# Performance work log

Hardware: AMD Instinct MI355X
Metric: run time of the kernel (lower is better)

## Reference

```python
import jax, jax.numpy as jnp
import numpy as np

D_ATTN = 64


def setup_inputs() -> dict:
    key = jax.random.key(0)
    ks = jax.random.split(key, 10)
    B, N, D_MODEL = 8, 1024, 512
    s = 0.02
    return {
        "x": jax.random.normal(ks[0], (B, N, D_MODEL), jnp.float32),
        "top": jax.random.normal(ks[1], (B, N, N, 16), jnp.float32),
        "Wq": jax.random.normal(ks[2], (D_MODEL, D_ATTN), jnp.float32) * s,
        "bq": jnp.zeros((D_ATTN,), jnp.float32),
        "Wk": jax.random.normal(ks[3], (D_MODEL, D_ATTN), jnp.float32) * s,
        "bk": jnp.zeros((D_ATTN,), jnp.float32),
        "Wv": jax.random.normal(ks[4], (D_MODEL, D_ATTN), jnp.float32) * s,
        "bv": jnp.zeros((D_ATTN,), jnp.float32),
        "Wt": jax.random.normal(ks[5], (16, 1), jnp.float32) * s,
        "bt": jnp.zeros((1,), jnp.float32),
    }


def reference(x, top, Wq, bq, Wk, bk, Wv, bv, Wt, bt):
    # QKV projections: [B,N,d_model] -> [B,N,d_attn]
    Q = x @ Wq + bq
    K = x @ Wk + bk
    V = x @ Wv + bv
    scale = 1.0 / jnp.sqrt(jnp.asarray(D_ATTN, x.dtype))
    # [B,N,N] attention logits
    logits = jnp.einsum("bnd,bmd->bnm", Q, K) * scale
    # learned topological bias: Linear(16,1) on [B,N,N,16] -> [B,N,N]
    bias = jnp.einsum("bnmf,fo->bnmo", top, Wt)[..., 0] + bt[0]
    score = jax.nn.softmax(logits + bias, axis=-1)
    return jnp.einsum("bnm,bmd->bnd", score, V)
```

## Files before the change

kernel.cpp:

```cpp
#include <hip/hip_runtime.h>
#include <hip/hip_bf16.h>

typedef __attribute__((ext_vector_type(8))) short short8;
typedef __attribute__((ext_vector_type(4))) float f32x4;
typedef unsigned short ushort_t;
typedef unsigned int uint_t;

#define D_MODEL 512
#define D_ATTN  64

__device__ __forceinline__ ushort_t f2bf(float f) {
    uint_t u = __float_as_uint(f);
    u += 0x7FFFu + ((u >> 16) & 1u);
    return (ushort_t)(u >> 16);
}
__device__ __forceinline__ f32x4 ntload4(const f32x4* p) {
    return __builtin_nontemporal_load(p);
}

__global__ __launch_bounds__(256)
void qkv_all(const float* __restrict__ x,
             const float* __restrict__ Wq, const float* __restrict__ bq,
             const float* __restrict__ Wk, const float* __restrict__ bk,
             const float* __restrict__ Wv, const float* __restrict__ bv,
             ushort_t* __restrict__ Q, ushort_t* __restrict__ K,
             ushort_t* __restrict__ Vt)
{
    const int l = threadIdx.x & 63, w = threadIdx.x >> 6;
    const size_t bn0 = (size_t)blockIdx.x << 4;
    const int r0 = w << 2;
    const float* xb = x + (bn0 + r0) * D_MODEL;
    { uintptr_t u = (uintptr_t)xb; asm volatile("" : "+v"(u)); xb = (const float*)u; }

    float aq[4] = {0,0,0,0}, ak[4] = {0,0,0,0}, av[4] = {0,0,0,0};
#pragma unroll 2
    for (int k = 0; k < D_MODEL; k += 4) {
        float4 xr[4];
#pragma unroll
        for (int r = 0; r < 4; ++r) xr[r] = *(const float4*)(xb + r * D_MODEL + k);
        float wqv[4], wkv[4], wvv[4];
#pragma unroll
        for (int kk = 0; kk < 4; ++kk) {
            wqv[kk] = Wq[(k + kk) * D_ATTN + l];
            wkv[kk] = Wk[(k + kk) * D_ATTN + l];
            wvv[kk] = Wv[(k + kk) * D_ATTN + l];
        }
#pragma unroll
        for (int r = 0; r < 4; ++r) {
            const float xv[4] = {xr[r].x, xr[r].y, xr[r].z, xr[r].w};
#pragma unroll
            for (int kk = 0; kk < 4; ++kk) {
                aq[r] = fmaf(xv[kk], wqv[kk], aq[r]);
                ak[r] = fmaf(xv[kk], wkv[kk], ak[r]);
                av[r] = fmaf(xv[kk], wvv[kk], av[r]);
            }
        }
    }
    const float bqv = bq[l], bkv = bk[l], bvv = bv[l];
#pragma unroll
    for (int r = 0; r < 4; ++r) {
        Q[(bn0 + r0 + r) * D_ATTN + l] = f2bf((aq[r] + bqv) * 0.125f);
        K[(bn0 + r0 + r) * D_ATTN + l] = f2bf(ak[r] + bkv);
    }
    const int b = (int)(bn0 >> 10), n0loc = (int)(bn0 & 1023);
    uint2 pv;
    pv.x = (uint_t)f2bf(av[0] + bvv) | ((uint_t)f2bf(av[1] + bvv) << 16);
    pv.y = (uint_t)f2bf(av[2] + bvv) | ((uint_t)f2bf(av[3] + bvv) << 16);
    *(uint2*)(Vt + ((size_t)(b * 64 + l) << 10) + n0loc + r0) = pv;
}

__global__ __launch_bounds__(256)
void topo_attn_f(const float* __restrict__ top, const float* __restrict__ Wt,
                 const ushort_t* __restrict__ Q, const ushort_t* __restrict__ K,
                 const ushort_t* __restrict__ Vt, float* __restrict__ out)
{
    __shared__ float lds[16384];
    const int tid = threadIdx.x;
    const int l = tid & 63, wv = tid >> 6;
    const int b   = blockIdx.x >> 6;
    const int bn0 = blockIdx.x << 4;

    {
        const f32x4* __restrict__ slab =
            (const f32x4*)top + ((size_t)bn0 << 12) + ((size_t)wv << 14) + l;
        const float4 wq = *(const float4*)(Wt + ((l & 3) << 2));
        const int mq = l >> 2;
        const bool sel0 = (l & 3) == 0;
#pragma unroll 1
        for (int bi = 0; bi < 16; ++bi) {
            f32x4 ld[16];
#pragma unroll
            for (int u = 0; u < 16; ++u)
                ld[u] = ntload4(slab + (((bi << 4) + u) << 6));
#pragma unroll
            for (int u = 0; u < 16; ++u) {
                int j = (bi << 4) + u;
                float p = ld[u][0] * wq.x;
                p = fmaf(ld[u][1], wq.y, p);
                p = fmaf(ld[u][2], wq.z, p);
                p = fmaf(ld[u][3], wq.w, p);
                p += __shfl_xor(p, 1);
                p += __shfl_xor(p, 2);
                int m_slab = (j << 4) + mq;
                int rloc = (wv << 2) + (m_slab >> 10);
                int m = m_slab & 1023;
                if (sel0) lds[rloc * 1024 + m] = p;
            }
        }
    }
    __syncthreads();

    const int lr = l & 15, lg = l >> 4;
    const short8 a0 = *(const short8*)(Q + ((size_t)(bn0 + lr)) * 64 + 8 * lg);
    const short8 a1 = *(const short8*)(Q + ((size_t)(bn0 + lr)) * 64 + 32 + 8 * lg);
    const ushort_t* __restrict__ Kb = K + ((size_t)b << 16);
#pragma unroll 4
    for (int t16 = 0; t16 < 16; ++t16) {
        int m0 = (wv << 8) + (t16 << 4);
        short8 kb0 = *(const short8*)(Kb + (size_t)(m0 + lr) * 64 + 8 * lg);
        short8 kb1 = *(const short8*)(Kb + (size_t)(m0 + lr) * 64 + 32 + 8 * lg);
        f32x4 acc = {0.f, 0.f, 0.f, 0.f};
        acc = __builtin_amdgcn_mfma_f32_16x16x32_bf16(a0, kb0, acc, 0, 0, 0);
        acc = __builtin_amdgcn_mfma_f32_16x16x32_bf16(a1, kb1, acc, 0, 0, 0);
#pragma unroll
        for (int j = 0; j < 4; ++j)
            lds[(4 * lg + j) * 1024 + m0 + lr] += acc[j];
    }
    __syncthreads();

    {
        const int r = tid >> 4, sseg = tid & 15;
        float4 v4[16];
        const float4* rowp = (const float4*)(lds + r * 1024 + sseg * 64);
#pragma unroll
        for (int i = 0; i < 16; ++i) v4[i] = rowp[i];
        __syncthreads();
        float mx = v4[0].x;
#pragma unroll
        for (int i = 0; i < 16; ++i)
            mx = fmaxf(mx, fmaxf(fmaxf(v4[i].x, v4[i].y), fmaxf(v4[i].z, v4[i].w)));
#pragma unroll
        for (int off = 8; off >= 1; off >>= 1) mx = fmaxf(mx, __shfl_xor(mx, off));
        float sum = 0.f;
#pragma unroll
        for (int i = 0; i < 16; ++i) {
            v4[i].x = __expf(v4[i].x - mx); sum += v4[i].x;
            v4[i].y = __expf(v4[i].y - mx); sum += v4[i].y;
            v4[i].z = __expf(v4[i].z - mx); sum += v4[i].z;
            v4[i].w = __expf(v4[i].w - mx); sum += v4[i].w;
        }
#pragma unroll
        for (int off = 8; off >= 1; off >>= 1) sum += __shfl_xor(sum, off);
        float inv = 1.0f / sum;
        ushort_t* pb = ((ushort_t*)lds) + r * 1024 + sseg * 64;
#pragma unroll
        for (int i = 0; i < 8; ++i) {
            uint_t w0 = (uint_t)f2bf(v4[2*i].x * inv)   | ((uint_t)f2bf(v4[2*i].y * inv)   << 16);
            uint_t w1 = (uint_t)f2bf(v4[2*i].z * inv)   | ((uint_t)f2bf(v4[2*i].w * inv)   << 16);
            uint_t w2 = (uint_t)f2bf(v4[2*i+1].x * inv) | ((uint_t)f2bf(v4[2*i+1].y * inv) << 16);
            uint_t w3 = (uint_t)f2bf(v4[2*i+1].z * inv) | ((uint_t)f2bf(v4[2*i+1].w * inv) << 16);
            ((uint4*)pb)[i] = make_uint4(w0, w1, w2, w3);
        }
    }
    __syncthreads();

    {
        f32x4 o[4] = {{0,0,0,0},{0,0,0,0},{0,0,0,0},{0,0,0,0}};
        const ushort_t* __restrict__ pb = ((const ushort_t*)lds) + lr * 1024;
        const ushort_t* __restrict__ Vb = Vt + ((size_t)b << 16);
#pragma unroll 2
        for (int c = 0; c < 8; ++c) {
            int m0 = (wv << 8) + (c << 5) + 8 * lg;
            short8 pa = *(const short8*)(pb + m0);
#pragma unroll
            for (int dt = 0; dt < 4; ++dt) {
                short8 vb = *(const short8*)(Vb + (size_t)(dt * 16 + lr) * 1024 + m0);
                o[dt] = __builtin_amdgcn_mfma_f32_16x16x32_bf16(pa, vb, o[dt], 0, 0, 0);
            }
        }
        float* lo = lds + 8192 + (wv << 10);
#pragma unroll
        for (int dt = 0; dt < 4; ++dt)
#pragma unroll
            for (int j = 0; j < 4; ++j)
                lo[(4 * lg + j) * 64 + dt * 16 + lr] = o[dt][j];
    }
    __syncthreads();

#pragma unroll
    for (int i = 0; i < 4; ++i) {
        int idx = (i << 8) + tid;
        float s2 = lds[8192 + idx] + lds[8192 + 1024 + idx]
                 + lds[8192 + 2048 + idx] + lds[8192 + 3072 + idx];
        out[((size_t)bn0 << 6) + idx] = s2;
    }
}

extern "C" void kernel_launch(void* const* d_in, const int* in_sizes, int n_in,
                              void* d_out, int out_size, void* d_ws, size_t ws_size,
                              hipStream_t stream) {
    const float* x   = (const float*)d_in[0];
    const float* top = (const float*)d_in[1];
    const float* Wq  = (const float*)d_in[2];
    const float* bq  = (const float*)d_in[3];
    const float* Wk  = (const float*)d_in[4];
    const float* bk  = (const float*)d_in[5];
    const float* Wv  = (const float*)d_in[6];
    const float* bv  = (const float*)d_in[7];
    const float* Wt  = (const float*)d_in[8];
    float* out = (float*)d_out;

    ushort_t* Q  = (ushort_t*)d_ws;
    ushort_t* K  = Q + 8 * 1024 * 64;
    ushort_t* Vt = K + 8 * 1024 * 64;

    qkv_all<<<512, 256, 0, stream>>>(x, Wq, bq, Wk, bk, Wv, bv, Q, K, Vt);
    topo_attn_f<<<512, 256, 0, stream>>>(top, Wt, Q, K, Vt, out);
}
```

Measured before the change: 161.0 us.

## Move topo bias reduction into QKV kernel with many blocks and bf16 bias buffer

The Linear(16,1) reduction over the 512 MB topology tensor moves out of the attention kernel into a fused first kernel. That kernel adds 4096 extra blocks, so the bandwidth-bound stream runs across far more workgroups than the previous 512, and it runs alongside the QKV projection blocks. The bias is written to workspace as bf16 and then loaded and widened into LDS by the attention kernel. This adds an extra global round trip of the bias and lowers its precision to bf16 before the softmax.

```diff
diff --git a/kernel.cpp b/kernel.cpp
--- a/kernel.cpp
+++ b/kernel.cpp
@@ -8,108 +8,124 @@
 
 #define D_MODEL 512
 #define D_ATTN  64
+#define BIAS_BLOCKS 4096
+#define QKV_BLOCKS  512
 
 __device__ __forceinline__ ushort_t f2bf(float f) {
     uint_t u = __float_as_uint(f);
     u += 0x7FFFu + ((u >> 16) & 1u);
     return (ushort_t)(u >> 16);
 }
+__device__ __forceinline__ float bf2f(ushort_t h) {
+    return __uint_as_float((uint_t)h << 16);
+}
 __device__ __forceinline__ f32x4 ntload4(const f32x4* p) {
     return __builtin_nontemporal_load(p);
 }
 
+__global__ __launch_bounds__(256, 6)
+void fused_bias_qkv(const float* __restrict__ x, const float* __restrict__ top,
+                    const float* __restrict__ Wq, const float* __restrict__ bq,
+                    const float* __restrict__ Wk, const float* __restrict__ bk,
+                    const float* __restrict__ Wv, const float* __restrict__ bv,
+                    const float* __restrict__ Wt,
+                    ushort_t* __restrict__ Q, ushort_t* __restrict__ K,
+                    ushort_t* __restrict__ Vt, ushort_t* __restrict__ bias)
+{
+    const int tid = threadIdx.x;
+    const int l = tid & 63, w = tid >> 6;
+
+    if (blockIdx.x < BIAS_BLOCKS) {
+        const int h   = (blockIdx.x << 2) + w;
+        const int row = h >> 1;
+        const int half = h & 1;
+        const f32x4* __restrict__ gp =
+            (const f32x4*)(top + ((size_t)row << 14) + ((size_t)half << 13)) + l;
+        ushort_t* __restrict__ op = bias + ((size_t)row << 10) + (half << 9);
+        const float4 wq = *(const float4*)(Wt + ((l & 3) << 2));
+        const int mq = l >> 2;
+        const bool sel0 = (l & 3) == 0;
+#pragma unroll 4
+        for (int it = 0; it < 32; ++it) {
+            f32x4 v = ntload4(gp + (it << 6));
+            float p = v[0] * wq.x;
+            p = fmaf(v[1], wq.y, p);
+            p = fmaf(v[2], wq.z, p);
+            p = fmaf(v[3], wq.w, p);
+            p += __shfl_xor(p, 1);
+            p += __shfl_xor(p, 2);
+            if (sel0) op[(it << 4) + mq] = f2bf(p);
+        }
+    } else {
+        const size_t bn0 = (size_t)(blockIdx.x - BIAS_BLOCKS) << 4;
+        const int r0 = w << 2;
+        const float* xb = x + (bn0 + r0) * D_MODEL;
+        { uintptr_t u = (uintptr_t)xb; asm volatile("" : "+v"(u)); xb = (const float*)u; }
+
+        float aq[4] = {0,0,0,0}, ak[4] = {0,0,0,0}, av[4] = {0,0,0,0};
+#pragma unroll 2
+        for (int k = 0; k < D_MODEL; k += 4) {
+            float4 xr[4];
+#pragma unroll
+            for (int r = 0; r < 4; ++r) xr[r] = *(const float4*)(xb + r * D_MODEL + k);
+            float wqv[4], wkv[4], wvv[4];
+#pragma unroll
+            for (int kk = 0; kk < 4; ++kk) {
+                wqv[kk] = Wq[(k + kk) * D_ATTN + l];
+                wkv[kk] = Wk[(k + kk) * D_ATTN + l];
+                wvv[kk] = Wv[(k + kk) * D_ATTN + l];
+            }
+#pragma unroll
+            for (int r = 0; r < 4; ++r) {
+                const float xv[4] = {xr[r].x, xr[r].y, xr[r].z, xr[r].w};
+#pragma unroll
+                for (int kk = 0; kk < 4; ++kk) {
+                    aq[r] = fmaf(xv[kk], wqv[kk], aq[r]);
+                    ak[r] = fmaf(xv[kk], wkv[kk], ak[r]);
+                    av[r] = fmaf(xv[kk], wvv[kk], av[r]);
+                }
+            }
+        }
+        const float bqv = bq[l], bkv = bk[l], bvv = bv[l];
+#pragma unroll
+        for (int r = 0; r < 4; ++r) {
+            Q[(bn0 + r0 + r) * D_ATTN + l] = f2bf((aq[r] + bqv) * 0.125f);
+            K[(bn0 + r0 + r) * D_ATTN + l] = f2bf(ak[r] + bkv);
+        }
+        const int b = (int)(bn0 >> 10), n0loc = (int)(bn0 & 1023);
+        uint2 pv;
+        pv.x = (uint_t)f2bf(av[0] + bvv) | ((uint_t)f2bf(av[1] + bvv) << 16);
+        pv.y = (uint_t)f2bf(av[2] + bvv) | ((uint_t)f2bf(av[3] + bvv) << 16);
+        *(uint2*)(Vt + ((size_t)(b * 64 + l) << 10) + n0loc + r0) = pv;
+    }
+}
+
 __global__ __launch_bounds__(256)
-void qkv_all(const float* __restrict__ x,
-             const float* __restrict__ Wq, const float* __restrict__ bq,
-             const float* __restrict__ Wk, const float* __restrict__ bk,
-             const float* __restrict__ Wv, const float* __restrict__ bv,
-             ushort_t* __restrict__ Q, ushort_t* __restrict__ K,
-             ushort_t* __restrict__ Vt)
-{
-    const int l = threadIdx.x & 63, w = threadIdx.x >> 6;
-    const size_t bn0 = (size_t)blockIdx.x << 4;
-    const int r0 = w << 2;
-    const float* xb = x + (bn0 + r0) * D_MODEL;
-    { uintptr_t u = (uintptr_t)xb; asm volatile("" : "+v"(u)); xb = (const float*)u; }
-
-    float aq[4] = {0,0,0,0}, ak[4] = {0,0,0,0}, av[4] = {0,0,0,0};
-#pragma unroll 2
-    for (int k = 0; k < D_MODEL; k += 4) {
-        float4 xr[4];
-#pragma unroll
-        for (int r = 0; r < 4; ++r) xr[r] = *(const float4*)(xb + r * D_MODEL + k);
-        float wqv[4], wkv[4], wvv[4];
-#pragma unroll
-        for (int kk = 0; kk < 4; ++kk) {
-            wqv[kk] = Wq[(k + kk) * D_ATTN + l];
-            wkv[kk] = Wk[(k + kk) * D_ATTN + l];
-            wvv[kk] = Wv[(k + kk) * D_ATTN + l];
-        }
-#pragma unroll
-        for (int r = 0; r < 4; ++r) {
-            const float xv[4] = {xr[r].x, xr[r].y, xr[r].z, xr[r].w};
-#pragma unroll
-            for (int kk = 0; kk < 4; ++kk) {
-                aq[r] = fmaf(xv[kk], wqv[kk], aq[r]);
-                ak[r] = fmaf(xv[kk], wkv[kk], ak[r]);
-                av[r] = fmaf(xv[kk], wvv[kk], av[r]);
-            }
-        }
-    }
-    const float bqv = bq[l], bkv = bk[l], bvv = bv[l];
-#pragma unroll
-    for (int r = 0; r < 4; ++r) {
-        Q[(bn0 + r0 + r) * D_ATTN + l] = f2bf((aq[r] + bqv) * 0.125f);
-        K[(bn0 + r0 + r) * D_ATTN + l] = f2bf(ak[r] + bkv);
-    }
-    const int b = (int)(bn0 >> 10), n0loc = (int)(bn0 & 1023);
-    uint2 pv;
-    pv.x = (uint_t)f2bf(av[0] + bvv) | ((uint_t)f2bf(av[1] + bvv) << 16);
-    pv.y = (uint_t)f2bf(av[2] + bvv) | ((uint_t)f2bf(av[3] + bvv) << 16);
-    *(uint2*)(Vt + ((size_t)(b * 64 + l) << 10) + n0loc + r0) = pv;
-}
-
-__global__ __launch_bounds__(256)
-void topo_attn_f(const float* __restrict__ top, const float* __restrict__ Wt,
-                 const ushort_t* __restrict__ Q, const ushort_t* __restrict__ K,
-                 const ushort_t* __restrict__ Vt, float* __restrict__ out)
+void topo_attn(const ushort_t* __restrict__ bias,
+               const ushort_t* __restrict__ Q, const ushort_t* __restrict__ K,
+               const ushort_t* __restrict__ Vt, float* __restrict__ out)
 {
     __shared__ float lds[16384];
     const int tid = threadIdx.x;
-    const int l = tid & 63, wv = tid >> 6;
     const int b   = blockIdx.x >> 6;
     const int bn0 = blockIdx.x << 4;
 
-    {
-        const f32x4* __restrict__ slab =
-            (const f32x4*)top + ((size_t)bn0 << 12) + ((size_t)wv << 14) + l;
-        const float4 wq = *(const float4*)(Wt + ((l & 3) << 2));
-        const int mq = l >> 2;
-        const bool sel0 = (l & 3) == 0;
-#pragma unroll 1
-        for (int bi = 0; bi < 16; ++bi) {
-            f32x4 ld[16];
-#pragma unroll
-            for (int u = 0; u < 16; ++u)
-                ld[u] = ntload4(slab + (((bi << 4) + u) << 6));
-#pragma unroll
-            for (int u = 0; u < 16; ++u) {
-                int j = (bi << 4) + u;
-                float p = ld[u][0] * wq.x;
-                p = fmaf(ld[u][1], wq.y, p);
-                p = fmaf(ld[u][2], wq.z, p);
-                p = fmaf(ld[u][3], wq.w, p);
-                p += __shfl_xor(p, 1);
-                p += __shfl_xor(p, 2);
-                int m_slab = (j << 4) + mq;
-                int rloc = (wv << 2) + (m_slab >> 10);
-                int m = m_slab & 1023;
-                if (sel0) lds[rloc * 1024 + m] = p;
-            }
-        }
-    }
-    __syncthreads();
-
+    const ushort_t* __restrict__ bb = bias + ((size_t)bn0 << 10);
+#pragma unroll
+    for (int it = 0; it < 8; ++it) {
+        int e0 = (it << 11) + (tid << 3);
+        short8 v = *(const short8*)(bb + e0);
+        f32x4 f0, f1;
+#pragma unroll
+        for (int j = 0; j < 4; ++j) f0[j] = bf2f((ushort_t)v[j]);
+#pragma unroll
+        for (int j = 0; j < 4; ++j) f1[j] = bf2f((ushort_t)v[4 + j]);
+        *(f32x4*)(lds + e0)     = f0;
+        *(f32x4*)(lds + e0 + 4) = f1;
+    }
+    __syncthreads();
+
+    const int l = tid & 63, wv = tid >> 6;
     const int lr = l & 15, lg = l >> 4;
     const short8 a0 = *(const short8*)(Q + ((size_t)(bn0 + lr)) * 64 + 8 * lg);
     const short8 a1 = *(const short8*)(Q + ((size_t)(bn0 + lr)) * 64 + 32 + 8 * lg);
@@ -210,10 +226,12 @@
     const float* Wt  = (const float*)d_in[8];
     float* out = (float*)d_out;
 
-    ushort_t* Q  = (ushort_t*)d_ws;
-    ushort_t* K  = Q + 8 * 1024 * 64;
-    ushort_t* Vt = K + 8 * 1024 * 64;
-
-    qkv_all<<<512, 256, 0, stream>>>(x, Wq, bq, Wk, bk, Wv, bv, Q, K, Vt);
-    topo_attn_f<<<512, 256, 0, stream>>>(top, Wt, Q, K, Vt, out);
-}
+    ushort_t* Q    = (ushort_t*)d_ws;
+    ushort_t* K    = Q + 8 * 1024 * 64;
+    ushort_t* Vt   = K + 8 * 1024 * 64;
+    ushort_t* bias = Vt + 8 * 1024 * 64;
+
+    fused_bias_qkv<<<BIAS_BLOCKS + QKV_BLOCKS, 256, 0, stream>>>(
+        x, top, Wq, bq, Wk, bk, Wv, bv, Wt, Q, K, Vt, bias);
+    topo_attn<<<512, 256, 0, stream>>>(bias, Q, K, Vt, out);
+}
```

Result: slower. 589.8 us (+266.4%).
